# Kernel tuning notes

Measured on AMD Instinct MI355X. Metric: run time of the kernel, lower is better.

Reference implementation:

```python
import math
import jax, jax.numpy as jnp
import numpy as np


def _skew(X, pad_value):
    # shift every row i one step right relative to row i-1: [B,M,L] -> [B,M,M+L]
    B, M, L = X.shape
    X = jnp.pad(X, ((0, 0), (0, 0), (0, M + 1)), constant_values=pad_value)
    X = X.reshape(B, -1)[:, :-M]
    return X.reshape(B, M, M + L)


def _unskew(X):
    # reverse of _skew: [B,M,M+L] -> [B,M,L]
    B, M, ML = X.shape
    L = ML - M
    X = X.reshape(B, -1)
    X = jnp.pad(X, ((0, 0), (0, M)))
    X = X.reshape(B, M, M + L + 1)
    return X[:, :, :L]


def setup_inputs() -> dict:
    key0 = jax.random.key(0)
    k1, k2, k3, k4 = jax.random.split(key0, 4)
    BH, M, D = 64, 1024, 64          # batch*heads, block len, head dim
    L = 1024                          # attn_span
    return {
        "query": jax.random.normal(k1, (BH, M, D), dtype=jnp.float32),
        "key": jax.random.normal(k2, (BH, M + L, D), dtype=jnp.float32),
        "value": jax.random.normal(k3, (BH, M + L, D), dtype=jnp.float32),
        "key_pe": jax.random.normal(k4, (1, D, L), dtype=jnp.float32),
    }


def reference(query, key, value, key_pe):
    hidden_size = query.shape[-1]
    # content scores: [BH, M, M+L] -> banded [BH, M, L]
    attn_cont = _unskew(jnp.matmul(query, jnp.swapaxes(key, -1, -2)))
    # relative position scores: [BH, M, L] (key_pe broadcasts over batch)
    attn_pos = jnp.matmul(query, key_pe)
    attn = (attn_cont + attn_pos) / math.sqrt(hidden_size)
    attn = jax.nn.softmax(attn, axis=-1)
    # dropout p=0.0 -> identity
    attn_skew = _skew(attn, 0.0)          # [BH, M, M+L]
    out = jnp.matmul(attn_skew, value)    # [BH, M, D]
    return out
```

## Files before the change

### kernel.cpp

```cpp
#include <hip/hip_runtime.h>
#include <hip/hip_bf16.h>


typedef __attribute__((ext_vector_type(8))) short bf16x8;
typedef __attribute__((ext_vector_type(4))) short bf16x4;
typedef __attribute__((ext_vector_type(4))) float f32x4;

#define BHN   64
#define MQ    1024
#define DH    64
#define LS    1024
#define NKEY  2048
#define NTILE 17

#define SZ_PE  ((size_t)LS * DH * 2)
#define OFF_K  SZ_PE
#define SZ_K   ((size_t)BHN * NKEY * DH * 2)
#define OFF_V  (OFF_K + SZ_K)
#define SZ_V   ((size_t)BHN * DH * NKEY * 2)
#define WS_NEED (OFF_V + SZ_V)

#define SCL_LOG2E 0.18033688011112042f

__device__ __forceinline__ short f2bf(float f) {
  unsigned u = __float_as_uint(f);
  u += 0x7FFFu + ((u >> 16) & 1u);
  return (short)(u >> 16);
}
__device__ __forceinline__ float bf2f(short s) {
  return __uint_as_float(((unsigned)(unsigned short)s) << 16);
}

#if defined(__has_builtin)
#if __has_builtin(__builtin_amdgcn_cvt_pk_bf16_f32)
#define HAVE_CVT_PK 1
#endif
#if __has_builtin(__builtin_amdgcn_exp2f)
#define HAVE_EXP2 1
#endif
#endif

__device__ __forceinline__ float fast_exp2(float x) {
#ifdef HAVE_EXP2
  return __builtin_amdgcn_exp2f(x);
#else
  return __builtin_exp2f(x);
#endif
}

__device__ __forceinline__ unsigned pk2(float a, float b) {
#ifdef HAVE_CVT_PK
  auto r = __builtin_amdgcn_cvt_pk_bf16_f32(a, b);
  unsigned u;
  __builtin_memcpy(&u, &r, 4);
  return u;
#else
  return (unsigned)(unsigned short)f2bf(a) | ((unsigned)(unsigned short)f2bf(b) << 16);
#endif
}
__device__ __forceinline__ bf16x4 mk4(unsigned a, unsigned b) {
  union { unsigned u[2]; bf16x4 v; } z;
  z.u[0] = a; z.u[1] = b;
  return z.v;
}
__device__ __forceinline__ bf16x8 mk8(unsigned a, unsigned b, unsigned c, unsigned d) {
  union { unsigned u[4]; bf16x8 v; } z;
  z.u[0] = a; z.u[1] = b; z.u[2] = c; z.u[3] = d;
  return z.v;
}
__device__ __forceinline__ void async_copy16(const void* g, void* l) {
  __builtin_amdgcn_global_load_lds((const __attribute__((address_space(1))) void*)g,
                                   (__attribute__((address_space(3))) void*)l, 16, 0, 0);
}

__global__ __launch_bounds__(256)
void prep_fused(const float* __restrict__ pe, const float* __restrict__ K,
                const float* __restrict__ V, short* __restrict__ peT,
                short* __restrict__ Kb, short* __restrict__ Vb) {
  __shared__ short st[64 * 68];
  const int bx = blockIdx.x;
  if (bx < 256) {
    const int idx = bx * 256 + threadIdx.x;
    const int rel = idx >> 6, d = idx & 63;
    peT[rel * 64 + (((d >> 3) ^ (rel & 7)) * 8) + (d & 7)] = f2bf(pe[d * LS + rel]);
  } else if (bx < 2304) {
    const size_t i = ((size_t)(bx - 256) * 256 + threadIdx.x) * 16;
    const int row = (int)(i >> 6);
    const int c16 = (int)(i & 63);
    const float4 f0 = *(const float4*)(K + i);
    const float4 f1 = *(const float4*)(K + i + 4);
    const float4 f2 = *(const float4*)(K + i + 8);
    const float4 f3 = *(const float4*)(K + i + 12);
    const bf16x8 b0 = mk8(pk2(f0.x, f0.y), pk2(f0.z, f0.w), pk2(f1.x, f1.y), pk2(f1.z, f1.w));
    const bf16x8 b1 = mk8(pk2(f2.x, f2.y), pk2(f2.z, f2.w), pk2(f3.x, f3.y), pk2(f3.z, f3.w));
    const int s7 = row & 7;
    short* dst = Kb + (size_t)row * 64;
    *(bf16x8*)&dst[(((c16 >> 3))     ^ s7) * 8] = b0;
    *(bf16x8*)&dst[(((c16 >> 3) + 1) ^ s7) * 8] = b1;
  } else {
    const int b  = bx - 2304;
    const int bh = b >> 5, jt = b & 31;
    {
      const int r = threadIdx.x >> 2, cb = (threadIdx.x & 3) * 16;
      const float* src = V + ((size_t)bh * NKEY + jt * 64 + r) * DH + cb;
#pragma unroll
      for (int c = 0; c < 16; c += 8) {
        float4 f0 = *(const float4*)(src + c);
        float4 f1 = *(const float4*)(src + c + 4);
        *(bf16x8*)&st[r * 68 + cb + c] =
            mk8(pk2(f0.x, f0.y), pk2(f0.z, f0.w), pk2(f1.x, f1.y), pk2(f1.z, f1.w));
      }
    }
    __syncthreads();
    {
      const int d = threadIdx.x >> 2, kapb = (threadIdx.x & 3) * 16;
      __attribute__((aligned(16))) short tmp[16];
#pragma unroll
      for (int j = 0; j < 16; ++j) {
        const int kap = kapb + j;
        const int k   = (kap & 3) * 16 + (kap >> 2);
        tmp[j] = st[k * 68 + d];
      }
      short* dst = Vb + ((size_t)bh * DH + d) * NKEY + jt * 64 + kapb;
      *(bf16x8*)dst       = *(bf16x8*)&tmp[0];
      *(bf16x8*)(dst + 8) = *(bf16x8*)&tmp[8];
    }
  }
}

template <bool PRECONV>
__global__ __launch_bounds__(256, 4)
void seq_attn_kernel(const float* __restrict__ Qf, const float* __restrict__ Kf,
                     const float* __restrict__ Vf, const short* __restrict__ peT,
                     const short* __restrict__ Kb, const short* __restrict__ Vb,
                     float* __restrict__ Out) {
  __shared__ short sK[64 * 64];
  __shared__ short sPE[2 * 64 * 64];
  __shared__ short sV[64 * 64];
  __shared__ short sPA[64 * 64];

  const int tid  = threadIdx.x;
  const int w    = tid >> 6;
  const int lane = tid & 63;
  const int li   = lane & 15;
  const int quad = lane >> 4;
  const int linear = blockIdx.y * 16 + blockIdx.x;
  const int slot   = linear >> 3;
  const int bh     = (linear & 7) * 8 + (slot >> 4);
  const int i0     = (slot & 15) * 64;
  const int rbase  = w * 16 + quad * 4;

  bf16x8 aq[2];
  {
    const float* qp = Qf + (size_t)((bh * MQ + i0 + w * 16 + li) * DH) + quad * 8;
#pragma unroll
    for (int ks = 0; ks < 2; ++ks) {
      float4 f0 = *(const float4*)(qp + ks * 32);
      float4 f1 = *(const float4*)(qp + ks * 32 + 4);
      f0.x *= SCL_LOG2E; f0.y *= SCL_LOG2E; f0.z *= SCL_LOG2E; f0.w *= SCL_LOG2E;
      f1.x *= SCL_LOG2E; f1.y *= SCL_LOG2E; f1.z *= SCL_LOG2E; f1.w *= SCL_LOG2E;
      aq[ks] = mk8(pk2(f0.x, f0.y), pk2(f0.z, f0.w), pk2(f1.x, f1.y), pk2(f1.z, f1.w));
    }
  }

  float l_i[4] = {0.f, 0.f, 0.f, 0.f};
  f32x4 acco[4];
#pragma unroll
  for (int nt = 0; nt < 4; ++nt) acco[nt] = (f32x4){0.f, 0.f, 0.f, 0.f};

  f32x4 curPw[4];
  f32x4 prevw3 = (f32x4){0.f, 0.f, 0.f, 0.f};

  for (int t = 0; t < NTILE; ++t) {
    const int j0 = i0 + t * 64;
    __syncthreads();

    if constexpr (PRECONV) {
      {
        const char* gb = (const char*)(Kb + ((size_t)bh * NKEY + j0) * 64);
#pragma unroll
        for (int it = 0; it < 2; ++it) {
          const int c0 = w * 128 + it * 64;
          async_copy16(gb + (size_t)(c0 + lane) * 16, (char*)sK + (size_t)c0 * 16);
        }
      }
      if (t < NTILE - 1) {
        const char* gb = (const char*)(peT + (size_t)t * 64 * 64);
        char* db = (char*)sPE + (size_t)(t & 1) * 8192;
#pragma unroll
        for (int it = 0; it < 2; ++it) {
          const int c0 = w * 128 + it * 64;
          async_copy16(gb + (size_t)(c0 + lane) * 16, db + (size_t)c0 * 16);
        }
      }
      {
#pragma unroll
        for (int it = 0; it < 2; ++it) {
          const int s = w * 128 + it * 64 + lane;
          const int d = s >> 3;
          const int g = (s & 7) ^ (d & 7);
          const short* gp = Vb + ((size_t)bh * DH + d) * NKEY + j0 + g * 8;
          async_copy16(gp, (char*)sV + (size_t)(w * 128 + it * 64) * 16);
        }
      }
    } else {
      {
        const int srow = tid >> 2, l0 = tid & 3, sdb = l0 * 16;
        const float* src = Kf + (size_t)(bh * NKEY + j0 + srow) * DH + sdb;
        const float4 a0 = *(const float4*)(src + 0);
        const float4 a1 = *(const float4*)(src + 4);
        const float4 a2 = *(const float4*)(src + 8);
        const float4 a3 = *(const float4*)(src + 12);
        const bf16x8 b0 = mk8(pk2(a0.x, a0.y), pk2(a0.z, a0.w), pk2(a1.x, a1.y), pk2(a1.z, a1.w));
        const bf16x8 b1 = mk8(pk2(a2.x, a2.y), pk2(a2.z, a2.w), pk2(a3.x, a3.y), pk2(a3.z, a3.w));
        const int s7 = srow & 7;
        *(bf16x8*)&sK[srow * 64 + (((2 * l0)     ^ s7) * 8)] = b0;
        *(bf16x8*)&sK[srow * 64 + (((2 * l0 + 1) ^ s7) * 8)] = b1;
      }
      {
        const int vdb = (tid & 15) * 4, vkb = (tid >> 4) * 4;
        const float* src = Vf + (size_t)(bh * NKEY + j0 + vkb) * DH + vdb;
#pragma unroll
        for (int m = 0; m < 4; ++m) {
          const float4 rr = *(const float4*)(src + m * DH);
          const int k   = vkb + m;
          const int kap = (k & 15) * 4 + (k >> 4);
#pragma unroll
          for (int jj = 0; jj < 4; ++jj) {
            const int d = vdb + jj;
            const float fv = (jj == 0) ? rr.x : (jj == 1) ? rr.y : (jj == 2) ? rr.z : rr.w;
            sV[d * 64 + (((kap >> 3) ^ (d & 7)) * 8) + (kap & 7)] = f2bf(fv);
          }
        }
      }
      if (t < NTILE - 1) {
        const short* src = peT + (size_t)t * 64 * 64;
        short* db = sPE + (size_t)(t & 1) * 4096;
        *(bf16x8*)&db[tid * 16]     = *(const bf16x8*)(src + tid * 16);
        *(bf16x8*)&db[tid * 16 + 8] = *(const bf16x8*)(src + tid * 16 + 8);
      }
    }
    __syncthreads();

#pragma unroll
    for (int m = 0; m < 4; ++m) {
      const int colIdx = 4 * t - w + m;
      const int base = ((colIdx >> 2) & 1) * 4096 + ((colIdx & 3) * 16 + li) * 64;
      f32x4 c = (f32x4){0.f, 0.f, 0.f, 0.f};
#pragma unroll
      for (int ks = 0; ks < 2; ++ks) {
        const int gs = (((ks * 4 + quad) ^ (li & 7)) * 8);
        const bf16x8 b = *(bf16x8*)&sPE[base + gs];
        c = __builtin_amdgcn_mfma_f32_16x16x32_bf16(aq[ks], b, c, 0, 0, 0);
      }
      curPw[m] = c;
    }

    f32x4 cs[4];
#pragma unroll
    for (int nt = 0; nt < 4; ++nt) {
      f32x4 c = (f32x4){0.f, 0.f, 0.f, 0.f};
#pragma unroll
      for (int ks = 0; ks < 2; ++ks) {
        const int gs = (((ks * 4 + quad) ^ (li & 7)) * 8);
        const bf16x8 b = *(bf16x8*)&sK[(nt * 16 + li) * 64 + gs];
        c = __builtin_amdgcn_mfma_f32_16x16x32_bf16(aq[ks], b, c, 0, 0, 0);
      }
      cs[nt] = c;
    }

#pragma unroll
    for (int r = 0; r < 4; ++r) {
      const int e       = li - quad * 4 - r;
      const bool ge     = (e >= 0);
      const int srcLane = quad * 16 + (e & 15);
      const float shm = __shfl(prevw3[r], srcLane);
      const unsigned pk01 = pk2(curPw[0][r], curPw[1][r]);
      const unsigned pk23 = pk2(curPw[2][r], curPw[3][r]);
      const unsigned s01 = (unsigned)__shfl((int)pk01, srcLane);
      const unsigned s23 = (unsigned)__shfl((int)pk23, srcLane);
      const float sh0 = bf2f((short)(s01 & 0xffffu));
      const float sh1 = bf2f((short)(s01 >> 16));
      const float sh2 = bf2f((short)(s23 & 0xffffu));
      const float sh3 = bf2f((short)(s23 >> 16));
      const float pos0 = ge ? sh0 : shm;
      const float pos1 = ge ? sh1 : sh0;
      const float pos2 = ge ? sh2 : sh1;
      const float pos3 = ge ? sh3 : sh2;
      float p0 = fast_exp2(cs[0][r] + pos0);
      float p1 = fast_exp2(cs[1][r] + pos1);
      float p2 = fast_exp2(cs[2][r] + pos2);
      float p3 = fast_exp2(cs[3][r] + pos3);
      if (t == 0) {
        p0 = (0 > w || (0 == w && ge)) ? p0 : 0.f;
        p1 = (1 > w || (1 == w && ge)) ? p1 : 0.f;
        p2 = (2 > w || (2 == w && ge)) ? p2 : 0.f;
        p3 = (3 > w || (3 == w && ge)) ? p3 : 0.f;
      } else if (t == NTILE - 1) {
        p0 = (0 < w || (0 == w && !ge)) ? p0 : 0.f;
        p1 = (1 < w || (1 == w && !ge)) ? p1 : 0.f;
        p2 = (2 < w || (2 == w && !ge)) ? p2 : 0.f;
        p3 = (3 < w || (3 == w && !ge)) ? p3 : 0.f;
      }
      l_i[r] += (p0 + p1) + (p2 + p3);
      const int rowA = rbase + r;
      const bf16x4 pkv = mk4(pk2(p0, p1), pk2(p2, p3));
      *(bf16x4*)&sPA[rowA * 64 + (((li >> 1) ^ (rowA & 7)) * 8) + (li & 1) * 4] = pkv;
    }
    prevw3 = curPw[3];

#pragma unroll
    for (int ks = 0; ks < 2; ++ks) {
      const int rowA = w * 16 + li;
      const bf16x8 ap =
          *(bf16x8*)&sPA[rowA * 64 + (((ks * 4 + quad) ^ (rowA & 7)) * 8)];
#pragma unroll
      for (int nt = 0; nt < 4; ++nt) {
        const int d  = nt * 16 + li;
        const int gs = (((ks * 4 + quad) ^ (d & 7)) * 8);
        const bf16x8 bv = *(bf16x8*)&sV[d * 64 + gs];
        acco[nt] = __builtin_amdgcn_mfma_f32_16x16x32_bf16(ap, bv, acco[nt], 0, 0, 0);
      }
    }
  }

#pragma unroll
  for (int r = 0; r < 4; ++r) {
    float l = l_i[r];
    l += __shfl_xor(l, 1);
    l += __shfl_xor(l, 2);
    l += __shfl_xor(l, 4);
    l += __shfl_xor(l, 8);
    const float inv = 1.0f / l;
#pragma unroll
    for (int nt = 0; nt < 4; ++nt) {
      Out[(size_t)(bh * MQ + i0 + rbase + r) * DH + nt * 16 + li] = acco[nt][r] * inv;
    }
  }
}

extern "C" void kernel_launch(void* const* d_in, const int* in_sizes, int n_in,
                              void* d_out, int out_size, void* d_ws, size_t ws_size,
                              hipStream_t stream) {
  const float* q  = (const float*)d_in[0];
  const float* k  = (const float*)d_in[1];
  const float* v  = (const float*)d_in[2];
  const float* pe = (const float*)d_in[3];
  float* out = (float*)d_out;
  short* peT = (short*)d_ws;
  short* Kb  = (short*)((char*)d_ws + OFF_K);
  short* Vb  = (short*)((char*)d_ws + OFF_V);
  const bool preconv = ws_size >= WS_NEED;

  dim3 grid(MQ / 64, BHN);
  if (preconv) {
    prep_fused<<<4352, 256, 0, stream>>>(pe, k, v, peT, Kb, Vb);
    seq_attn_kernel<true><<<grid, 256, 0, stream>>>(q, k, v, peT, Kb, Vb, out);
  } else {
    prep_fused<<<256, 256, 0, stream>>>(pe, k, v, peT, Kb, Vb);
    seq_attn_kernel<false><<<grid, 256, 0, stream>>>(q, k, v, peT, Kb, Vb, out);
  }
}
```

Before: 172.3 us.

## Register-prefetch next K/PE/V tiles instead of synchronous direct-to-LDS copies

Replaces the per-tile global_load_lds async copies of K, positional-embedding and V tiles with register prefetching. The next tile is loaded into registers while the current tile is computed, then written to LDS at the start of the next iteration, so global latency overlaps with MFMA work. It also raises wave priority around the MFMA sections with s_setprio and swaps the trailing __syncthreads for an explicit lgkmcnt wait plus barrier. In exchange it uses more registers (six bf16x8 prefetch buffers) and adds explicit LDS store instructions.

```diff
diff --git a/kernel.cpp b/kernel.cpp
--- a/kernel.cpp
+++ b/kernel.cpp
@@ -67,10 +67,6 @@
   union { unsigned u[4]; bf16x8 v; } z;
   z.u[0] = a; z.u[1] = b; z.u[2] = c; z.u[3] = d;
   return z.v;
-}
-__device__ __forceinline__ void async_copy16(const void* g, void* l) {
-  __builtin_amdgcn_global_load_lds((const __attribute__((address_space(1))) void*)g,
-                                   (__attribute__((address_space(3))) void*)l, 16, 0, 0);
 }
 
 __global__ __launch_bounds__(256)
@@ -171,39 +167,55 @@
   f32x4 curPw[4];
   f32x4 prevw3 = (f32x4){0.f, 0.f, 0.f, 0.f};
 
+  bf16x8 pfK0, pfK1, pfP0, pfP1, pfV0, pfV1;
+  const short *pK, *pP, *pV0, *pV1;
+  if constexpr (PRECONV) {
+    pK = Kb + ((size_t)bh * NKEY + i0) * DH + tid * 8 + 1024;
+    pP = peT + tid * 8 + 1024;
+    const int d0 = tid >> 3;
+    const int g0 = (tid & 7) ^ (d0 & 7);
+    pV0 = Vb + ((size_t)bh * DH + d0) * NKEY + i0 + g0 * 8;
+    pV1 = pV0 + (size_t)32 * NKEY;
+    pfK0 = *(const bf16x8*)(pK - 1024);
+    pfK1 = *(const bf16x8*)(pK + 1024);
+    pfP0 = *(const bf16x8*)(pP - 1024);
+    pfP1 = *(const bf16x8*)(pP + 1024);
+    pfV0 = *(const bf16x8*)(pV0);
+    pfV1 = *(const bf16x8*)(pV1);
+    pK += 4096; pP += 4096; pV0 += 64; pV1 += 64;
+  }
+
   for (int t = 0; t < NTILE; ++t) {
-    const int j0 = i0 + t * 64;
     __syncthreads();
 
     if constexpr (PRECONV) {
-      {
-        const char* gb = (const char*)(Kb + ((size_t)bh * NKEY + j0) * 64);
-#pragma unroll
-        for (int it = 0; it < 2; ++it) {
-          const int c0 = w * 128 + it * 64;
-          async_copy16(gb + (size_t)(c0 + lane) * 16, (char*)sK + (size_t)c0 * 16);
+      *(bf16x8*)&sK[tid * 8]        = pfK0;
+      *(bf16x8*)&sK[tid * 8 + 2048] = pfK1;
+      if (t < NTILE - 1) {
+        short* pe = sPE + (t & 1) * 4096;
+        *(bf16x8*)&pe[tid * 8]        = pfP0;
+        *(bf16x8*)&pe[tid * 8 + 2048] = pfP1;
+      }
+      *(bf16x8*)&sV[tid * 8]        = pfV0;
+      *(bf16x8*)&sV[tid * 8 + 2048] = pfV1;
+      if (t + 1 < NTILE) {
+        pfK0 = *(const bf16x8*)(pK - 1024);
+        pfK1 = *(const bf16x8*)(pK + 1024);
+        pfV0 = *(const bf16x8*)(pV0);
+        pfV1 = *(const bf16x8*)(pV1);
+        pK += 4096; pV0 += 64; pV1 += 64;
+        if (t + 1 < NTILE - 1) {
+          pfP0 = *(const bf16x8*)(pP - 1024);
+          pfP1 = *(const bf16x8*)(pP + 1024);
+          pP += 4096;
         }
       }
-      if (t < NTILE - 1) {
-        const char* gb = (const char*)(peT + (size_t)t * 64 * 64);
-        char* db = (char*)sPE + (size_t)(t & 1) * 8192;
-#pragma unroll
-        for (int it = 0; it < 2; ++it) {
-          const int c0 = w * 128 + it * 64;
-          async_copy16(gb + (size_t)(c0 + lane) * 16, db + (size_t)c0 * 16);
-        }
-      }
-      {
-#pragma unroll
-        for (int it = 0; it < 2; ++it) {
-          const int s = w * 128 + it * 64 + lane;
-          const int d = s >> 3;
-          const int g = (s & 7) ^ (d & 7);
-          const short* gp = Vb + ((size_t)bh * DH + d) * NKEY + j0 + g * 8;
-          async_copy16(gp, (char*)sV + (size_t)(w * 128 + it * 64) * 16);
-        }
-      }
+      asm volatile("s_waitcnt lgkmcnt(0)" ::: "memory");
+      __builtin_amdgcn_sched_barrier(0);
+      __builtin_amdgcn_s_barrier();
+      __builtin_amdgcn_sched_barrier(0);
     } else {
+      const int j0 = i0 + t * 64;
       {
         const int srow = tid >> 2, l0 = tid & 3, sdb = l0 * 16;
         const float* src = Kf + (size_t)(bh * NKEY + j0 + srow) * DH + sdb;
@@ -239,9 +251,10 @@
         *(bf16x8*)&db[tid * 16]     = *(const bf16x8*)(src + tid * 16);
         *(bf16x8*)&db[tid * 16 + 8] = *(const bf16x8*)(src + tid * 16 + 8);
       }
-    }
-    __syncthreads();
-
+      __syncthreads();
+    }
+
+    __builtin_amdgcn_s_setprio(1);
 #pragma unroll
     for (int m = 0; m < 4; ++m) {
       const int colIdx = 4 * t - w + m;
@@ -268,6 +281,7 @@
       }
       cs[nt] = c;
     }
+    __builtin_amdgcn_s_setprio(0);
 
 #pragma unroll
     for (int r = 0; r < 4; ++r) {
@@ -309,6 +323,7 @@
     }
     prevw3 = curPw[3];
 
+    __builtin_amdgcn_s_setprio(1);
 #pragma unroll
     for (int ks = 0; ks < 2; ++ks) {
       const int rowA = w * 16 + li;
@@ -322,6 +337,7 @@
         acco[nt] = __builtin_amdgcn_mfma_f32_16x16x32_bf16(ap, bv, acco[nt], 0, 0, 0);
       }
     }
+    __builtin_amdgcn_s_setprio(0);
   }
 
 #pragma unroll
```

New measurement: 171.3 us. About the same (-0.6%).

## Load K/V/PE MFMA operands directly from global, drop LDS staging and barriers

Applied to the files above, without the earlier changes.

In the preconverted path, each wave now loads its K, positional-embedding and V MFMA fragments straight from global memory into registers instead of staging them in shared memory. Only the softmax probability tile stays in LDS, and it is wave-private, so the per-tile block barriers are removed and LDS use drops to 8 KB. Wave priority is raised around the MFMA sections. The trade is that every wave re-reads the whole K/V tile from cache (four times the global traffic per block), and load latency is no longer hidden by a shared prefetch.

```diff
diff --git a/kernel.cpp b/kernel.cpp
--- a/kernel.cpp
+++ b/kernel.cpp
@@ -67,10 +67,6 @@
   union { unsigned u[4]; bf16x8 v; } z;
   z.u[0] = a; z.u[1] = b; z.u[2] = c; z.u[3] = d;
   return z.v;
-}
-__device__ __forceinline__ void async_copy16(const void* g, void* l) {
-  __builtin_amdgcn_global_load_lds((const __attribute__((address_space(1))) void*)g,
-                                   (__attribute__((address_space(3))) void*)l, 16, 0, 0);
 }
 
 __global__ __launch_bounds__(256)
@@ -134,10 +130,11 @@
                      const float* __restrict__ Vf, const short* __restrict__ peT,
                      const short* __restrict__ Kb, const short* __restrict__ Vb,
                      float* __restrict__ Out) {
-  __shared__ short sK[64 * 64];
-  __shared__ short sPE[2 * 64 * 64];
-  __shared__ short sV[64 * 64];
-  __shared__ short sPA[64 * 64];
+  __shared__ short smem[PRECONV ? 4096 : 16384];
+  short* const sP  = smem;
+  short* const sK  = smem;
+  short* const sPE = smem + 4096;
+  short* const sV  = smem + 12288;
 
   const int tid  = threadIdx.x;
   const int w    = tid >> 6;
@@ -171,39 +168,21 @@
   f32x4 curPw[4];
   f32x4 prevw3 = (f32x4){0.f, 0.f, 0.f, 0.f};
 
+  const int gsq0 = ((0 * 4 + quad) ^ (li & 7)) * 8;
+  const int gsq1 = ((1 * 4 + quad) ^ (li & 7)) * 8;
+  const short* pkl = (const short*)nullptr;
+  const short* pvl = (const short*)nullptr;
+  const short* ppl = (const short*)nullptr;
+  if constexpr (PRECONV) {
+    pkl = Kb + ((size_t)bh * NKEY + i0 + li) * 64;
+    pvl = Vb + ((size_t)bh * DH + li) * NKEY + i0 + quad * 8;
+    ppl = peT + (size_t)li * 64;
+  }
+
   for (int t = 0; t < NTILE; ++t) {
-    const int j0 = i0 + t * 64;
-    __syncthreads();
-
-    if constexpr (PRECONV) {
-      {
-        const char* gb = (const char*)(Kb + ((size_t)bh * NKEY + j0) * 64);
-#pragma unroll
-        for (int it = 0; it < 2; ++it) {
-          const int c0 = w * 128 + it * 64;
-          async_copy16(gb + (size_t)(c0 + lane) * 16, (char*)sK + (size_t)c0 * 16);
-        }
-      }
-      if (t < NTILE - 1) {
-        const char* gb = (const char*)(peT + (size_t)t * 64 * 64);
-        char* db = (char*)sPE + (size_t)(t & 1) * 8192;
-#pragma unroll
-        for (int it = 0; it < 2; ++it) {
-          const int c0 = w * 128 + it * 64;
-          async_copy16(gb + (size_t)(c0 + lane) * 16, db + (size_t)c0 * 16);
-        }
-      }
-      {
-#pragma unroll
-        for (int it = 0; it < 2; ++it) {
-          const int s = w * 128 + it * 64 + lane;
-          const int d = s >> 3;
-          const int g = (s & 7) ^ (d & 7);
-          const short* gp = Vb + ((size_t)bh * DH + d) * NKEY + j0 + g * 8;
-          async_copy16(gp, (char*)sV + (size_t)(w * 128 + it * 64) * 16);
-        }
-      }
-    } else {
+    if constexpr (!PRECONV) {
+      __syncthreads();
+      const int j0 = i0 + t * 64;
       {
         const int srow = tid >> 2, l0 = tid & 3, sdb = l0 * 16;
         const float* src = Kf + (size_t)(bh * NKEY + j0 + srow) * DH + sdb;
@@ -239,36 +218,76 @@
         *(bf16x8*)&db[tid * 16]     = *(const bf16x8*)(src + tid * 16);
         *(bf16x8*)&db[tid * 16 + 8] = *(const bf16x8*)(src + tid * 16 + 8);
       }
-    }
-    __syncthreads();
-
-#pragma unroll
-    for (int m = 0; m < 4; ++m) {
-      const int colIdx = 4 * t - w + m;
-      const int base = ((colIdx >> 2) & 1) * 4096 + ((colIdx & 3) * 16 + li) * 64;
-      f32x4 c = (f32x4){0.f, 0.f, 0.f, 0.f};
-#pragma unroll
-      for (int ks = 0; ks < 2; ++ks) {
-        const int gs = (((ks * 4 + quad) ^ (li & 7)) * 8);
-        const bf16x8 b = *(bf16x8*)&sPE[base + gs];
-        c = __builtin_amdgcn_mfma_f32_16x16x32_bf16(aq[ks], b, c, 0, 0, 0);
-      }
-      curPw[m] = c;
+      __syncthreads();
+    }
+
+    __builtin_amdgcn_s_setprio(1);
+    if constexpr (PRECONV) {
+      bf16x8 fp0[4], fp1[4];
+#pragma unroll
+      for (int m = 0; m < 4; ++m) {
+        int cidx = 4 * t - w + m;
+        cidx = cidx < 0 ? 0 : (cidx > 63 ? 63 : cidx);
+        const short* p = ppl + cidx * 1024;
+        fp0[m] = *(const bf16x8*)(p + gsq0);
+        fp1[m] = *(const bf16x8*)(p + gsq1);
+      }
+#pragma unroll
+      for (int m = 0; m < 4; ++m) {
+        f32x4 c = (f32x4){0.f, 0.f, 0.f, 0.f};
+        c = __builtin_amdgcn_mfma_f32_16x16x32_bf16(aq[0], fp0[m], c, 0, 0, 0);
+        c = __builtin_amdgcn_mfma_f32_16x16x32_bf16(aq[1], fp1[m], c, 0, 0, 0);
+        curPw[m] = c;
+      }
+    } else {
+#pragma unroll
+      for (int m = 0; m < 4; ++m) {
+        const int colIdx = 4 * t - w + m;
+        const int base = ((colIdx >> 2) & 1) * 4096 + ((colIdx & 3) * 16 + li) * 64;
+        f32x4 c = (f32x4){0.f, 0.f, 0.f, 0.f};
+#pragma unroll
+        for (int ks = 0; ks < 2; ++ks) {
+          const int gs = (((ks * 4 + quad) ^ (li & 7)) * 8);
+          const bf16x8 b = *(bf16x8*)&sPE[base + gs];
+          c = __builtin_amdgcn_mfma_f32_16x16x32_bf16(aq[ks], b, c, 0, 0, 0);
+        }
+        curPw[m] = c;
+      }
     }
 
     f32x4 cs[4];
-#pragma unroll
-    for (int nt = 0; nt < 4; ++nt) {
-      f32x4 c = (f32x4){0.f, 0.f, 0.f, 0.f};
-#pragma unroll
-      for (int ks = 0; ks < 2; ++ks) {
-        const int gs = (((ks * 4 + quad) ^ (li & 7)) * 8);
-        const bf16x8 b = *(bf16x8*)&sK[(nt * 16 + li) * 64 + gs];
-        c = __builtin_amdgcn_mfma_f32_16x16x32_bf16(aq[ks], b, c, 0, 0, 0);
-      }
-      cs[nt] = c;
-    }
-
+    if constexpr (PRECONV) {
+      bf16x8 fk0[4], fk1[4];
+      const int tb = t * 4096;
+#pragma unroll
+      for (int nt = 0; nt < 4; ++nt) {
+        const short* p = pkl + tb + nt * 1024;
+        fk0[nt] = *(const bf16x8*)(p + gsq0);
+        fk1[nt] = *(const bf16x8*)(p + gsq1);
+      }
+#pragma unroll
+      for (int nt = 0; nt < 4; ++nt) {
+        f32x4 c = (f32x4){0.f, 0.f, 0.f, 0.f};
+        c = __builtin_amdgcn_mfma_f32_16x16x32_bf16(aq[0], fk0[nt], c, 0, 0, 0);
+        c = __builtin_amdgcn_mfma_f32_16x16x32_bf16(aq[1], fk1[nt], c, 0, 0, 0);
+        cs[nt] = c;
+      }
+    } else {
+#pragma unroll
+      for (int nt = 0; nt < 4; ++nt) {
+        f32x4 c = (f32x4){0.f, 0.f, 0.f, 0.f};
+#pragma unroll
+        for (int ks = 0; ks < 2; ++ks) {
+          const int gs = (((ks * 4 + quad) ^ (li & 7)) * 8);
+          const bf16x8 b = *(bf16x8*)&sK[(nt * 16 + li) * 64 + gs];
+          c = __builtin_amdgcn_mfma_f32_16x16x32_bf16(aq[ks], b, c, 0, 0, 0);
+        }
+        cs[nt] = c;
+      }
+    }
+    __builtin_amdgcn_s_setprio(0);
+
+    bf16x4 pkv[4];
 #pragma unroll
     for (int r = 0; r < 4; ++r) {
       const int e       = li - quad * 4 - r;
@@ -303,25 +322,50 @@
         p3 = (3 < w || (3 == w && !ge)) ? p3 : 0.f;
       }
       l_i[r] += (p0 + p1) + (p2 + p3);
+      pkv[r] = mk4(pk2(p0, p1), pk2(p2, p3));
+    }
+    prevw3 = curPw[3];
+
+    short* const pbuf = PRECONV ? sP : sK;
+#pragma unroll
+    for (int r = 0; r < 4; ++r) {
       const int rowA = rbase + r;
-      const bf16x4 pkv = mk4(pk2(p0, p1), pk2(p2, p3));
-      *(bf16x4*)&sPA[rowA * 64 + (((li >> 1) ^ (rowA & 7)) * 8) + (li & 1) * 4] = pkv;
-    }
-    prevw3 = curPw[3];
-
-#pragma unroll
-    for (int ks = 0; ks < 2; ++ks) {
+      *(bf16x4*)&pbuf[rowA * 64 + (((li >> 1) ^ (rowA & 7)) * 8) + (li & 1) * 4] = pkv[r];
+    }
+
+    __builtin_amdgcn_s_setprio(1);
+    if constexpr (PRECONV) {
+      bf16x8 fv0[4], fv1[4];
+#pragma unroll
+      for (int nt = 0; nt < 4; ++nt) {
+        const short* p = pvl + nt * (16 * NKEY) + t * 64;
+        fv0[nt] = *(const bf16x8*)(p);
+        fv1[nt] = *(const bf16x8*)(p + 32);
+      }
       const int rowA = w * 16 + li;
-      const bf16x8 ap =
-          *(bf16x8*)&sPA[rowA * 64 + (((ks * 4 + quad) ^ (rowA & 7)) * 8)];
+      const bf16x8 ap0 = *(bf16x8*)&sP[rowA * 64 + (((0 * 4 + quad) ^ (rowA & 7)) * 8)];
+      const bf16x8 ap1 = *(bf16x8*)&sP[rowA * 64 + (((1 * 4 + quad) ^ (rowA & 7)) * 8)];
 #pragma unroll
       for (int nt = 0; nt < 4; ++nt) {
-        const int d  = nt * 16 + li;
-        const int gs = (((ks * 4 + quad) ^ (d & 7)) * 8);
-        const bf16x8 bv = *(bf16x8*)&sV[d * 64 + gs];
-        acco[nt] = __builtin_amdgcn_mfma_f32_16x16x32_bf16(ap, bv, acco[nt], 0, 0, 0);
-      }
-    }
+        acco[nt] = __builtin_amdgcn_mfma_f32_16x16x32_bf16(ap0, fv0[nt], acco[nt], 0, 0, 0);
+        acco[nt] = __builtin_amdgcn_mfma_f32_16x16x32_bf16(ap1, fv1[nt], acco[nt], 0, 0, 0);
+      }
+    } else {
+#pragma unroll
+      for (int ks = 0; ks < 2; ++ks) {
+        const int rowA = w * 16 + li;
+        const bf16x8 ap =
+            *(bf16x8*)&sK[rowA * 64 + (((ks * 4 + quad) ^ (rowA & 7)) * 8)];
+#pragma unroll
+        for (int nt = 0; nt < 4; ++nt) {
+          const int d  = nt * 16 + li;
+          const int gs = (((ks * 4 + quad) ^ (d & 7)) * 8);
+          const bf16x8 bv = *(bf16x8*)&sV[d * 64 + gs];
+          acco[nt] = __builtin_amdgcn_mfma_f32_16x16x32_bf16(ap, bv, acco[nt], 0, 0, 0);
+        }
+      }
+    }
+    __builtin_amdgcn_s_setprio(0);
   }
 
 #pragma unroll
```

New measurement: 223.2 us. +29.5%, slower.
